# Performance work log

Hardware: AMD Instinct MI355X
Metric: run time of the kernel (lower is better)

Reference implementation:

```python
import jax, jax.numpy as jnp
import numpy as np

NN_SIZE = 10


def batch_normals(x, k=NN_SIZE):
    """x: (B, 3, N) NCHW point cloud -> per-point normals (B, 3, N).

    kNN (including self) -> local covariance -> smallest eigenvector.
    """
    pts = jnp.transpose(x, (0, 2, 1))  # (B, N, 3)
    sq = jnp.sum(pts * pts, axis=-1)  # (B, N)
    # pairwise squared distances (B, N, N); the inner product is a big GEMM
    d2 = sq[:, :, None] + sq[:, None, :] - 2.0 * jnp.einsum('bnd,bmd->bnm', pts, pts)
    _, idx = jax.lax.top_k(-d2, k)  # (B, N, k) nearest neighbors (incl. self)
    nbrs = jax.vmap(lambda p, i: p[i])(pts, idx)  # (B, N, k, 3)
    centered = nbrs - jnp.mean(nbrs, axis=2, keepdims=True)
    cov = jnp.einsum('bnki,bnkj->bnij', centered, centered) / k  # (B, N, 3, 3)
    _, vecs = jnp.linalg.eigh(cov)  # eigenvalues ascending
    normal = vecs[..., :, 0]  # eigenvector of smallest eigenvalue, (B, N, 3)
    return jnp.transpose(normal, (0, 2, 1))  # (B, 3, N)


def setup_inputs() -> dict:
    key = jax.random.key(0)
    k1, k2 = jax.random.split(key)
    pred = jax.random.normal(k1, (8, 3, 4096), dtype=jnp.float32)
    gt = jax.random.normal(k2, (8, 3, 4096), dtype=jnp.float32)
    return {"pred": pred, "gt": gt}


def reference(pred, gt):
    pred_normals = batch_normals(pred)
    gt_normals = batch_normals(gt)
    # metric = "mse"
    return jnp.mean((pred_normals - gt_normals) ** 2)
```

## Files before the change

### kernel.cpp

```cpp
#include <hip/hip_runtime.h>
#include <math.h>

#define NPTS 4096
#define KNN 10
#define CAP 48
#define TAU_SLACK 1e-4f
#define NRM_N (8 * 3 * NPTS)
#define DYN_BYTES (NPTS * 16 + 128 * CAP * 2 + 512)

__device__ __forceinline__ float med3f(float a, float b, float c) {
    return __builtin_amdgcn_fmed3f(a, b, c);
}


__device__ __forceinline__ float slapy2_(float x, float y) {
    float ax = fabsf(x), ay = fabsf(y);
    float w = fmaxf(ax, ay), z = fminf(ax, ay);
    if (z == 0.f) return w;
    float t = z / w;
    return w * sqrtf(1.f + t * t);
}

__device__ __forceinline__ void slartg_(float f, float g, float* c, float* s, float* r) {
    if (g == 0.f) { *c = 1.f; *s = 0.f; *r = f; }
    else if (f == 0.f) { *c = 0.f; *s = copysignf(1.f, g); *r = fabsf(g); }
    else {
        float f1 = fabsf(f);
        float d = sqrtf(f * f + g * g);
        float rr = copysignf(d, f);
        *c = f1 / d;
        *s = g / rr;
        *r = rr;
    }
}

__device__ void slaev2_(float a, float b, float c,
                        float* rt1, float* rt2, float* cs1, float* sn1) {
    float sm = a + c;
    float df = a - c;
    float adf = fabsf(df);
    float tb = b + b;
    float ab = fabsf(tb);
    float acmx, acmn;
    if (fabsf(a) > fabsf(c)) { acmx = a; acmn = c; } else { acmx = c; acmn = a; }
    float rt;
    if (adf > ab)      { float t = ab / adf; rt = adf * sqrtf(1.f + t * t); }
    else if (adf < ab) { float t = adf / ab; rt = ab * sqrtf(1.f + t * t); }
    else               { rt = ab * sqrtf(2.f); }
    int sgn1;
    if (sm < 0.f) {
        *rt1 = 0.5f * (sm - rt); sgn1 = -1;
        *rt2 = (acmx / *rt1) * acmn - (b / *rt1) * b;
    } else if (sm > 0.f) {
        *rt1 = 0.5f * (sm + rt); sgn1 = 1;
        *rt2 = (acmx / *rt1) * acmn - (b / *rt1) * b;
    } else {
        *rt1 = 0.5f * rt; *rt2 = -0.5f * rt; sgn1 = 1;
    }
    int sgn2;
    float cs;
    if (df >= 0.f) { cs = df + rt; sgn2 = 1; } else { cs = df - rt; sgn2 = -1; }
    float acs = fabsf(cs);
    if (acs > ab) {
        float ct = -tb / cs;
        *sn1 = 1.f / sqrtf(1.f + ct * ct);
        *cs1 = ct * (*sn1);
    } else {
        if (ab == 0.f) { *cs1 = 1.f; *sn1 = 0.f; }
        else {
            float tn = -cs / tb;
            *cs1 = 1.f / sqrtf(1.f + tn * tn);
            *sn1 = tn * (*cs1);
        }
    }
    if (sgn1 == sgn2) { float tn = *cs1; *cs1 = -(*sn1); *sn1 = tn; }
}

__device__ void steqr3_(float* d, float* e, float Z[3][3]) {
    const float eps    = 5.9604644775390625e-8f;
    const float eps2   = eps * eps;
    const float safmin = 1.17549435e-38f;
    const int n = 3, nm1 = 2;
    const int nmaxit = 90;
    int jtot = 0, l1 = 1;
    int guard = 0;

    while (l1 <= n) {
        if (++guard > 600) break;
        if (l1 > 1) e[l1 - 2] = 0.f;
        int m = n;
        if (l1 <= nm1) {
            for (int mm = l1; mm <= nm1; ++mm) {
                float tst = fabsf(e[mm - 1]);
                if (tst == 0.f) { m = mm; break; }
                if (tst <= (sqrtf(fabsf(d[mm - 1])) * sqrtf(fabsf(d[mm]))) * eps) {
                    e[mm - 1] = 0.f; m = mm; break;
                }
            }
        }
        int l = l1, lsv = l1, lend = m, lendsv = m;
        l1 = m + 1;
        if (lend == l) continue;
        float anorm = 0.f;
        for (int i = l; i <= lend; i++) anorm = fmaxf(anorm, fabsf(d[i - 1]));
        for (int i = l; i <= lend - 1; i++) anorm = fmaxf(anorm, fabsf(e[i - 1]));
        if (anorm == 0.f) continue;
        if (fabsf(d[lend - 1]) < fabsf(d[l - 1])) { lend = lsv; l = lendsv; }

        if (lend > l) {
            for (;;) {
                if (++guard > 600) return;
                int m2 = lend;
                if (l != lend) {
                    for (int mm = l; mm <= lend - 1; ++mm) {
                        float tst = e[mm - 1] * e[mm - 1];
                        if (tst <= (eps2 * fabsf(d[mm - 1])) * fabsf(d[mm]) + safmin) { m2 = mm; break; }
                    }
                }
                if (m2 < lend) e[m2 - 1] = 0.f;
                float p = d[l - 1];
                if (m2 == l) {
                    d[l - 1] = p; l = l + 1;
                    if (l <= lend) continue;
                    break;
                }
                if (m2 == l + 1) {
                    float rt1, rt2, c, s;
                    slaev2_(d[l - 1], e[l - 1], d[l], &rt1, &rt2, &c, &s);
                    for (int i = 0; i < 3; i++) {
                        float t = Z[i][l];
                        Z[i][l]     = c * t - s * Z[i][l - 1];
                        Z[i][l - 1] = s * t + c * Z[i][l - 1];
                    }
                    d[l - 1] = rt1; d[l] = rt2; e[l - 1] = 0.f;
                    l += 2;
                    if (l <= lend) continue;
                    break;
                }
                if (jtot == nmaxit) break;
                jtot++;
                float g = (d[l] - p) / (2.f * e[l - 1]);
                float r = slapy2_(g, 1.f);
                g = d[m2 - 1] - p + e[l - 1] / (g + copysignf(r, g));
                float s = 1.f, c = 1.f;
                p = 0.f;
                float csv[2], snv[2];
                for (int i = m2 - 1; i >= l; --i) {
                    float f = s * e[i - 1];
                    float b = c * e[i - 1];
                    slartg_(g, f, &c, &s, &r);
                    if (i != m2 - 1) e[i] = r;
                    g = d[i] - p;
                    r = (d[i - 1] - g) * s + 2.f * c * b;
                    p = s * r;
                    d[i] = g + p;
                    g = c * r - b;
                    csv[i - l] = c; snv[i - l] = -s;
                }
                int nrot = m2 - l;
                for (int j = nrot; j >= 1; --j) {
                    float C = csv[j - 1], S = snv[j - 1];
                    for (int i = 0; i < 3; i++) {
                        float t = Z[i][l - 1 + j];
                        Z[i][l - 1 + j] = C * t - S * Z[i][l - 2 + j];
                        Z[i][l - 2 + j] = S * t + C * Z[i][l - 2 + j];
                    }
                }
                d[l - 1] = d[l - 1] - p;
                e[l - 1] = g;
            }
        } else {
            for (;;) {
                if (++guard > 600) return;
                int m2 = lend;
                if (l != lend) {
                    for (int mm = l; mm >= lend + 1; --mm) {
                        float tst = e[mm - 2] * e[mm - 2];
                        if (tst <= (eps2 * fabsf(d[mm - 1])) * fabsf(d[mm - 2]) + safmin) { m2 = mm; break; }
                    }
                }
                if (m2 > lend) e[m2 - 2] = 0.f;
                float p = d[l - 1];
                if (m2 == l) {
                    d[l - 1] = p; l = l - 1;
                    if (l >= lend) continue;
                    break;
                }
                if (m2 == l - 1) {
                    float rt1, rt2, c, s;
                    slaev2_(d[l - 2], e[l - 2], d[l - 1], &rt1, &rt2, &c, &s);
                    for (int i = 0; i < 3; i++) {
                        float t = Z[i][l - 1];
                        Z[i][l - 1] = c * t - s * Z[i][l - 2];
                        Z[i][l - 2] = s * t + c * Z[i][l - 2];
                    }
                    d[l - 2] = rt1; d[l - 1] = rt2; e[l - 2] = 0.f;
                    l -= 2;
                    if (l >= lend) continue;
                    break;
                }
                if (jtot == nmaxit) break;
                jtot++;
                float g = (d[l - 2] - p) / (2.f * e[l - 2]);
                float r = slapy2_(g, 1.f);
                g = d[m2 - 1] - p + e[l - 2] / (g + copysignf(r, g));
                float s = 1.f, c = 1.f;
                p = 0.f;
                float csv[2], snv[2];
                for (int i = m2; i <= l - 1; ++i) {
                    float f = s * e[i - 1];
                    float b = c * e[i - 1];
                    slartg_(g, f, &c, &s, &r);
                    if (i != m2) e[i - 2] = r;
                    g = d[i - 1] - p;
                    r = (d[i] - g) * s + 2.f * c * b;
                    p = s * r;
                    d[i - 1] = g + p;
                    g = c * r - b;
                    csv[i - m2] = c; snv[i - m2] = s;
                }
                int nrot = l - m2;
                for (int j = 1; j <= nrot; ++j) {
                    float C = csv[j - 1], S = snv[j - 1];
                    for (int i = 0; i < 3; i++) {
                        float t = Z[i][m2 - 1 + j];
                        Z[i][m2 - 1 + j] = C * t - S * Z[i][m2 - 2 + j];
                        Z[i][m2 - 2 + j] = S * t + C * Z[i][m2 - 2 + j];
                    }
                }
                d[l - 1] -= p;
                e[l - 2] = g;
            }
        }
    }
    for (int ii = 2; ii <= n; ++ii) {
        int i = ii - 1, k = i;
        float p = d[i - 1];
        for (int j = ii; j <= n; ++j) {
            if (d[j - 1] < p) { k = j; p = d[j - 1]; }
        }
        if (k != i) {
            d[k - 1] = d[i - 1]; d[i - 1] = p;
            for (int r2 = 0; r2 < 3; r2++) {
                float t = Z[r2][i - 1]; Z[r2][i - 1] = Z[r2][k - 1]; Z[r2][k - 1] = t;
            }
        }
    }
}

__device__ void eig_normal3(const float xs[KNN], const float ys[KNN], const float zs[KNN],
                            float out[3]) {
    float mx = 0.f, my = 0.f, mz = 0.f;
#pragma unroll
    for (int s = 0; s < KNN; s++) { mx += xs[s]; my += ys[s]; mz += zs[s]; }
    mx /= 10.0f; my /= 10.0f; mz /= 10.0f;

    float c00 = 0.f, c10 = 0.f, c20 = 0.f, c11 = 0.f, c21 = 0.f, c22 = 0.f;
#pragma unroll
    for (int s = 0; s < KNN; s++) {
        float dx = xs[s] - mx, dy = ys[s] - my, dz = zs[s] - mz;
        c00 = fmaf(dx, dx, c00);
        c10 = fmaf(dy, dx, c10);
        c20 = fmaf(dz, dx, c20);
        c11 = fmaf(dy, dy, c11);
        c21 = fmaf(dz, dy, c21);
        c22 = fmaf(dz, dz, c22);
    }
    c00 /= 10.0f; c10 /= 10.0f; c20 /= 10.0f; c11 /= 10.0f; c21 /= 10.0f; c22 /= 10.0f;

    float alpha = c10, x2 = c20;
    float tau, v2, beta;
    float xnorm = fabsf(x2);
    if (xnorm == 0.f) { tau = 0.f; v2 = 0.f; beta = alpha; }
    else {
        beta = -copysignf(slapy2_(alpha, xnorm), alpha);
        tau = (beta - alpha) / beta;
        v2 = x2 / (alpha - beta);
    }
    float d[3], e[2];
    d[0] = c00;
    if (tau != 0.f) {
        float p0 = tau * (c11 + c21 * v2);
        float p1 = tau * (c21 + c22 * v2);
        float aw = -0.5f * tau * (p0 + p1 * v2);
        float w0 = p0 + aw;
        float w1 = p1 + aw * v2;
        d[1] = (c11 - w0) - w0;
        e[1] = (c21 - v2 * w0) - w1;
        d[2] = (c22 - v2 * w1) - w1 * v2;
        e[0] = beta;
    } else {
        d[1] = c11; d[2] = c22; e[0] = beta; e[1] = c21;
    }

    float Z[3][3] = {{1.f, 0.f, 0.f}, {0.f, 1.f, 0.f}, {0.f, 0.f, 1.f}};
    steqr3_(d, e, Z);

    float y0 = Z[0][0], y1 = Z[1][0], y2 = Z[2][0];
    if (tau != 0.f) {
        float t = tau * (y1 + v2 * y2);
        y1 = y1 - t;
        y2 = y2 - t * v2;
    }
    out[0] = y0; out[1] = y1; out[2] = y2;
}

__device__ __forceinline__ void merge_round(float* v, int off) {
    float t[KNN];
#pragma unroll
    for (int i = 0; i < KNN; i++) t[i] = fminf(v[i], __shfl_xor(v[KNN - 1 - i], off));
#define CE(a, b) { float hi = fmaxf(t[a], t[b]); float lo = fminf(t[a], t[b]); t[a] = hi; t[b] = lo; }
    CE(0, 8) CE(1, 9)
    CE(0, 4) CE(1, 5) CE(2, 6) CE(3, 7)
    CE(0, 2) CE(1, 3) CE(4, 6) CE(5, 7)
    CE(0, 1) CE(2, 3) CE(4, 5) CE(6, 7) CE(8, 9)
#undef CE
#pragma unroll
    for (int i = 0; i < KNN; i++) v[i] = t[i];
}

__device__ void do_phase4(const float* __restrict__ src, int chunk, int tid,
                          float4* pts, unsigned short* spairs, int* scnt,
                          float nv[3]) {
    for (int j = tid; j < NPTS; j += 512) {
        float x = src[j], y = src[NPTS + j], z = src[2 * NPTS + j];
        float w = fmaf(z, z, fmaf(y, y, x * x));
        pts[j] = make_float4(x, y, z, w);
    }
    if (tid < 128) scnt[tid] = 0;
    __syncthreads();

    int part = tid & 15;
    int qg = tid >> 4;
    int ql0 = qg * 4;
    int q0 = chunk * 128 + ql0;

    float m2x[4], m2y[4], m2z[4];
#pragma unroll
    for (int c = 0; c < 4; c++) {
        float4 p = pts[q0 + c];
        m2x[c] = -2.f * p.x; m2y[c] = -2.f * p.y; m2z[c] = -2.f * p.z;
    }

    float v[4][KNN + 1];
#pragma unroll
    for (int c = 0; c < 4; c++) {
#pragma unroll
        for (int s = 0; s < KNN; s++) v[c][s] = INFINITY;
        v[c][KNN] = -INFINITY;
    }

#pragma unroll 2
    for (int g = 0; g < 32; g++) {
        int jb = part + 128 * g;
        float m[4] = {INFINITY, INFINITY, INFINITY, INFINITY};
#pragma unroll
        for (int u = 0; u < 8; u++) {
            float4 p = pts[jb + 16 * u];
#pragma unroll
            for (int c = 0; c < 4; c++) {
                float key = fmaf(m2z[c], p.z, fmaf(m2y[c], p.y, fmaf(m2x[c], p.x, p.w)));
                m[c] = fminf(m[c], key);
            }
        }
#pragma unroll
        for (int c = 0; c < 4; c++)
#pragma unroll
            for (int s = 0; s < KNN; s++) v[c][s] = med3f(m[c], v[c][s], v[c][s + 1]);
    }

    float tauS[4];
#pragma unroll
    for (int c = 0; c < 4; c++) {
        merge_round(v[c], 1);
        merge_round(v[c], 2);
        merge_round(v[c], 4);
        merge_round(v[c], 8);
        tauS[c] = v[c][0] + TAU_SLACK;
    }

#pragma unroll 2
    for (int mm = 0; mm < 256; mm++) {
        int j = part + 16 * mm;
        float4 p = pts[j];
#pragma unroll
        for (int c = 0; c < 4; c++) {
            float key = fmaf(m2z[c], p.z, fmaf(m2y[c], p.y, fmaf(m2x[c], p.x, p.w)));
            if (key <= tauS[c]) {
                int ql = ql0 + c;
                int pos = atomicAdd(&scnt[ql], 1);
                if (pos < CAP) spairs[ql * CAP + pos] = (unsigned short)j;
            }
        }
    }
    __syncthreads();

    if (tid < 128) {
        int ql = tid;
        int qi = chunk * 128 + ql;
        float4 q = pts[qi];
        float qw = q.w;
        int cnt = scnt[ql];

        float bd[KNN]; int bi_[KNN];
#pragma unroll
        for (int s = 0; s < KNN; s++) { bd[s] = 3.4e38f; bi_[s] = 0; }
        float worst = 3.4e38f;
        int wslot = 0;
        if (cnt > CAP) {
            for (int j = 0; j < NPTS; j++) {
                float4 p = pts[j];
                float dot = fmaf(q.z, p.z, fmaf(q.y, p.y, q.x * p.x));
                float d2 = (qw + p.w) - 2.f * dot;
                if (d2 < worst) {
#pragma unroll
                    for (int s = 0; s < KNN; s++) { if (s == wslot) { bd[s] = d2; bi_[s] = j; } }
                    float wm = bd[0]; int ws = 0;
#pragma unroll
                    for (int s = 1; s < KNN; s++) { if (bd[s] > wm) { wm = bd[s]; ws = s; } }
                    worst = wm; wslot = ws;
                }
            }
        } else {
            for (int t = 0; t < cnt; t++) {
                int j = spairs[ql * CAP + t];
                float4 p = pts[j];
                float dot = fmaf(q.z, p.z, fmaf(q.y, p.y, q.x * p.x));
                float d2 = (qw + p.w) - 2.f * dot;
                if (d2 < worst) {
#pragma unroll
                    for (int s = 0; s < KNN; s++) { if (s == wslot) { bd[s] = d2; bi_[s] = j; } }
                    float wm = bd[0]; int ws = 0;
#pragma unroll
                    for (int s = 1; s < KNN; s++) { if (bd[s] > wm) { wm = bd[s]; ws = s; } }
                    worst = wm; wslot = ws;
                }
            }
        }
#pragma unroll
        for (int a = 0; a < KNN - 1; a++)
#pragma unroll
            for (int b2 = 0; b2 < KNN - 1 - a; b2++) {
                bool sw = (bd[b2] > bd[b2 + 1]) ||
                          (bd[b2] == bd[b2 + 1] && bi_[b2] > bi_[b2 + 1]);
                float d_lo = sw ? bd[b2 + 1] : bd[b2];
                float d_hi = sw ? bd[b2] : bd[b2 + 1];
                int   i_lo = sw ? bi_[b2 + 1] : bi_[b2];
                int   i_hi = sw ? bi_[b2] : bi_[b2 + 1];
                bd[b2] = d_lo; bd[b2 + 1] = d_hi; bi_[b2] = i_lo; bi_[b2 + 1] = i_hi;
            }
        float xs[KNN], ys[KNN], zs[KNN];
#pragma unroll
        for (int s = 0; s < KNN; s++) {
            float4 p = pts[bi_[s]];
            xs[s] = p.x; ys[s] = p.y; zs[s] = p.z;
        }
        eig_normal3(xs, ys, zs, nv);
    }
    __syncthreads();
}

__global__ __launch_bounds__(512, 4) void normals4_kernel(const float* __restrict__ pred,
                                                          const float* __restrict__ gt,
                                                          float* __restrict__ nrm,
                                                          float* __restrict__ out) {
    extern __shared__ char dynlds[];
    float4* pts = (float4*)dynlds;
    unsigned short* spairs = (unsigned short*)(dynlds + NPTS * 16);
    int* scnt = (int*)(dynlds + NPTS * 16 + 128 * CAP * 2);

    int tid = threadIdx.x;
    int bid = blockIdx.x;
    if (bid == 0 && tid == 0) out[0] = 0.f;
    int cloud = bid >> 8;
    int b = (bid >> 5) & 7;
    int chunk = bid & 31;

    const float* src = (cloud == 0 ? pred : gt) + (size_t)b * 3 * NPTS;
    float nv[3] = {0.f, 0.f, 0.f};
    do_phase4(src, chunk, tid, pts, spairs, scnt, nv);

    if (tid < 128) {
        int qg2 = chunk * 128 + tid;
        float* dst = nrm + ((size_t)cloud * 8 + b) * 3 * NPTS;
        dst[0 * NPTS + qg2] = nv[0];
        dst[1 * NPTS + qg2] = nv[1];
        dst[2 * NPTS + qg2] = nv[2];
    }
}

__global__ __launch_bounds__(256) void loss_kernel(const float* __restrict__ nrm,
                                                   float* __restrict__ out) {
    const int n = NRM_N;
    const float* a = nrm;
    const float* b = nrm + n;
    float acc = 0.f;
    for (int i = blockIdx.x * 256 + threadIdx.x; i < n; i += gridDim.x * 256) {
        float dd = a[i] - b[i];
        acc = fmaf(dd, dd, acc);
    }
#pragma unroll
    for (int off = 32; off > 0; off >>= 1) acc += __shfl_down(acc, off);
    __shared__ float wsum[4];
    int lane = threadIdx.x & 63, wv = threadIdx.x >> 6;
    if (lane == 0) wsum[wv] = acc;
    __syncthreads();
    if (threadIdx.x == 0) {
        float t = wsum[0] + wsum[1] + wsum[2] + wsum[3];
        atomicAdd(out, t * (1.f / (float)n));
    }
}

extern "C" void kernel_launch(void* const* d_in, const int* in_sizes, int n_in,
                              void* d_out, int out_size, void* d_ws, size_t ws_size,
                              hipStream_t stream) {
    (void)in_sizes; (void)n_in; (void)out_size; (void)ws_size;
    const float* pred = (const float*)d_in[0];
    const float* gt   = (const float*)d_in[1];
    float* out = (float*)d_out;
    float* nrm = (float*)d_ws;

    hipFuncSetAttribute(
        reinterpret_cast<const void*>(normals4_kernel),
        hipFuncAttributeMaxDynamicSharedMemorySize, DYN_BYTES);

    hipLaunchKernelGGL(normals4_kernel, dim3(512), dim3(512), DYN_BYTES, stream,
                       pred, gt, nrm, out);
    hipLaunchKernelGGL(loss_kernel, dim3(96), dim3(256), 0, stream, nrm, out);
}
```

Baseline: 170.2 us.

## Fuse loss into normals kernel, processing pred and gt per block with 64-query chunks

Each block now handles 64 queries from the same batch for both the pred and gt clouds, computing both normals in turn. It then reduces the squared difference in-register and adds it atomically to the output. This removes the workspace write and the separate loss kernel launch. The cost is that each block reloads the 4096-point cloud twice. Each query is also split over 32 threads instead of 16, which needs one more merge round.

```diff
diff --git a/kernel.cpp b/kernel.cpp
--- a/kernel.cpp
+++ b/kernel.cpp
@@ -5,8 +5,8 @@
 #define KNN 10
 #define CAP 48
 #define TAU_SLACK 1e-4f
-#define NRM_N (8 * 3 * NPTS)
-#define DYN_BYTES (NPTS * 16 + 128 * CAP * 2 + 512)
+#define QC 64
+#define DYN_BYTES (NPTS * 16 + QC * CAP * 2 + 256)
 
 __device__ __forceinline__ float med3f(float a, float b, float c) {
     return __builtin_amdgcn_fmed3f(a, b, c);
@@ -319,21 +319,21 @@
     for (int i = 0; i < KNN; i++) v[i] = t[i];
 }
 
-__device__ void do_phase4(const float* __restrict__ src, int chunk, int tid,
-                          float4* pts, unsigned short* spairs, int* scnt,
-                          float nv[3]) {
+__device__ void do_phase64(const float* __restrict__ src, int chunk, int tid,
+                           float4* pts, unsigned short* spairs, int* scnt,
+                           float nv[3]) {
     for (int j = tid; j < NPTS; j += 512) {
         float x = src[j], y = src[NPTS + j], z = src[2 * NPTS + j];
         float w = fmaf(z, z, fmaf(y, y, x * x));
         pts[j] = make_float4(x, y, z, w);
     }
-    if (tid < 128) scnt[tid] = 0;
+    if (tid < QC) scnt[tid] = 0;
     __syncthreads();
 
-    int part = tid & 15;
-    int qg = tid >> 4;
+    int part = tid & 31;
+    int qg = tid >> 5;
     int ql0 = qg * 4;
-    int q0 = chunk * 128 + ql0;
+    int q0 = chunk * QC + ql0;
 
     float m2x[4], m2y[4], m2z[4];
 #pragma unroll
@@ -351,12 +351,12 @@
     }
 
 #pragma unroll 2
-    for (int g = 0; g < 32; g++) {
-        int jb = part + 128 * g;
+    for (int g = 0; g < 16; g++) {
+        int jb = part + 256 * g;
         float m[4] = {INFINITY, INFINITY, INFINITY, INFINITY};
 #pragma unroll
         for (int u = 0; u < 8; u++) {
-            float4 p = pts[jb + 16 * u];
+            float4 p = pts[jb + 32 * u];
 #pragma unroll
             for (int c = 0; c < 4; c++) {
                 float key = fmaf(m2z[c], p.z, fmaf(m2y[c], p.y, fmaf(m2x[c], p.x, p.w)));
@@ -376,12 +376,13 @@
         merge_round(v[c], 2);
         merge_round(v[c], 4);
         merge_round(v[c], 8);
+        merge_round(v[c], 16);
         tauS[c] = v[c][0] + TAU_SLACK;
     }
 
 #pragma unroll 2
-    for (int mm = 0; mm < 256; mm++) {
-        int j = part + 16 * mm;
+    for (int mm = 0; mm < 128; mm++) {
+        int j = part + 32 * mm;
         float4 p = pts[j];
 #pragma unroll
         for (int c = 0; c < 4; c++) {
@@ -395,9 +396,9 @@
     }
     __syncthreads();
 
-    if (tid < 128) {
+    if (tid < QC) {
         int ql = tid;
-        int qi = chunk * 128 + ql;
+        int qi = chunk * QC + ql;
         float4 q = pts[qi];
         float qw = q.w;
         int cnt = scnt[ql];
@@ -460,71 +461,48 @@
     __syncthreads();
 }
 
-__global__ __launch_bounds__(512, 4) void normals4_kernel(const float* __restrict__ pred,
-                                                          const float* __restrict__ gt,
-                                                          float* __restrict__ nrm,
-                                                          float* __restrict__ out) {
+__global__ __launch_bounds__(512, 4) void fused64_kernel(const float* __restrict__ pred,
+                                                         const float* __restrict__ gt,
+                                                         float* __restrict__ out) {
     extern __shared__ char dynlds[];
     float4* pts = (float4*)dynlds;
     unsigned short* spairs = (unsigned short*)(dynlds + NPTS * 16);
-    int* scnt = (int*)(dynlds + NPTS * 16 + 128 * CAP * 2);
+    int* scnt = (int*)(dynlds + NPTS * 16 + QC * CAP * 2);
 
     int tid = threadIdx.x;
     int bid = blockIdx.x;
-    if (bid == 0 && tid == 0) out[0] = 0.f;
-    int cloud = bid >> 8;
-    int b = (bid >> 5) & 7;
-    int chunk = bid & 31;
-
-    const float* src = (cloud == 0 ? pred : gt) + (size_t)b * 3 * NPTS;
-    float nv[3] = {0.f, 0.f, 0.f};
-    do_phase4(src, chunk, tid, pts, spairs, scnt, nv);
-
-    if (tid < 128) {
-        int qg2 = chunk * 128 + tid;
-        float* dst = nrm + ((size_t)cloud * 8 + b) * 3 * NPTS;
-        dst[0 * NPTS + qg2] = nv[0];
-        dst[1 * NPTS + qg2] = nv[1];
-        dst[2 * NPTS + qg2] = nv[2];
-    }
-}
-
-__global__ __launch_bounds__(256) void loss_kernel(const float* __restrict__ nrm,
-                                                   float* __restrict__ out) {
-    const int n = NRM_N;
-    const float* a = nrm;
-    const float* b = nrm + n;
-    float acc = 0.f;
-    for (int i = blockIdx.x * 256 + threadIdx.x; i < n; i += gridDim.x * 256) {
-        float dd = a[i] - b[i];
-        acc = fmaf(dd, dd, acc);
-    }
-#pragma unroll
-    for (int off = 32; off > 0; off >>= 1) acc += __shfl_down(acc, off);
-    __shared__ float wsum[4];
-    int lane = threadIdx.x & 63, wv = threadIdx.x >> 6;
-    if (lane == 0) wsum[wv] = acc;
-    __syncthreads();
-    if (threadIdx.x == 0) {
-        float t = wsum[0] + wsum[1] + wsum[2] + wsum[3];
-        atomicAdd(out, t * (1.f / (float)n));
+    int b = bid >> 6;
+    int chunk = bid & 63;
+
+    const float* pbase = pred + (size_t)b * 3 * NPTS;
+    const float* gbase = gt + (size_t)b * 3 * NPTS;
+
+    float va[3] = {0.f, 0.f, 0.f}, vb[3] = {0.f, 0.f, 0.f};
+    do_phase64(pbase, chunk, tid, pts, spairs, scnt, va);
+    do_phase64(gbase, chunk, tid, pts, spairs, scnt, vb);
+
+    if (tid < QC) {
+        float d0 = va[0] - vb[0], d1 = va[1] - vb[1], d2 = va[2] - vb[2];
+        float acc = fmaf(d2, d2, fmaf(d1, d1, d0 * d0));
+#pragma unroll
+        for (int off = 32; off > 0; off >>= 1) acc += __shfl_down(acc, off);
+        if (tid == 0) atomicAdd(out, acc * (1.f / (float)(8 * 3 * NPTS)));
     }
 }
 
 extern "C" void kernel_launch(void* const* d_in, const int* in_sizes, int n_in,
                               void* d_out, int out_size, void* d_ws, size_t ws_size,
                               hipStream_t stream) {
-    (void)in_sizes; (void)n_in; (void)out_size; (void)ws_size;
+    (void)in_sizes; (void)n_in; (void)d_ws; (void)ws_size;
     const float* pred = (const float*)d_in[0];
     const float* gt   = (const float*)d_in[1];
     float* out = (float*)d_out;
-    float* nrm = (float*)d_ws;
 
     hipFuncSetAttribute(
-        reinterpret_cast<const void*>(normals4_kernel),
+        reinterpret_cast<const void*>(fused64_kernel),
         hipFuncAttributeMaxDynamicSharedMemorySize, DYN_BYTES);
 
-    hipLaunchKernelGGL(normals4_kernel, dim3(512), dim3(512), DYN_BYTES, stream,
-                       pred, gt, nrm, out);
-    hipLaunchKernelGGL(loss_kernel, dim3(96), dim3(256), 0, stream, nrm, out);
-}
+    hipMemsetAsync(d_out, 0, (size_t)out_size * sizeof(float), stream);
+    hipLaunchKernelGGL(fused64_kernel, dim3(512), dim3(512), DYN_BYTES, stream,
+                       pred, gt, out);
+}
```

Result: slower. 205.6 us (+20.8%).
